# Kernel tuning notes

Hardware: AMD Instinct MI355X
Metric: run time of the kernel (lower is better)

The kernel has to match this reference:

```python
import jax, jax.numpy as jnp
import numpy as np

B, S, H = 64, 1024, 512
EPS = 1e-5


def layer_norm(x, g, b):
    mu = jnp.mean(x, axis=-1, keepdims=True)
    var = jnp.mean(jnp.square(x - mu), axis=-1, keepdims=True)
    return (x - mu) * jax.lax.rsqrt(var + EPS) * g + b


def lstm(x, w_ih, w_hh, b_ih, b_hh):
    # x: [B,S,H]; gates order (PyTorch): i, f, g, o; w_*: [4H, H]
    gx = jnp.einsum('bsh,gh->bsg', x, w_ih) + b_ih + b_hh  # [B,S,4H] one big GEMM
    gx = jnp.swapaxes(gx, 0, 1)  # time-major [S,B,4H]
    h0 = jnp.zeros((x.shape[0], w_hh.shape[1]), x.dtype)

    def step(carry, g_t):
        h, c = carry
        g = g_t + h @ w_hh.T
        i, f, gg, o = jnp.split(g, 4, axis=-1)
        c = jax.nn.sigmoid(f) * c + jax.nn.sigmoid(i) * jnp.tanh(gg)
        h = jax.nn.sigmoid(o) * jnp.tanh(c)
        return (h, c), h

    _, hs = jax.lax.scan(step, (h0, h0), gx)
    return jnp.swapaxes(hs, 0, 1)  # [B,S,H]


def setup_inputs() -> dict:
    key = jax.random.key(0)
    ks = jax.random.split(key, 12)
    s = 1.0 / np.sqrt(H)  # matches torch default uniform(-1/sqrt(H), 1/sqrt(H)) scale
    return {
        'x': jax.random.normal(ks[0], (B, S, H), jnp.float32),
        'pre_g': jnp.ones((H,), jnp.float32),
        'pre_b': jnp.zeros((H,), jnp.float32),
        'w_ih': jax.random.uniform(ks[1], (4 * H, H), jnp.float32, -s, s),
        'w_hh': jax.random.uniform(ks[2], (4 * H, H), jnp.float32, -s, s),
        'b_ih': jax.random.uniform(ks[3], (4 * H,), jnp.float32, -s, s),
        'b_hh': jax.random.uniform(ks[4], (4 * H,), jnp.float32, -s, s),
        'post_g': jnp.ones((H,), jnp.float32),
        'post_b': jnp.zeros((H,), jnp.float32),
        'w1': jax.random.uniform(ks[5], (H, 2 * H), jnp.float32, -s, s),
        'b1': jax.random.uniform(ks[6], (2 * H,), jnp.float32, -s, s),
        'w2': jax.random.uniform(ks[7], (2 * H, H), jnp.float32, -1.0 / np.sqrt(2 * H), 1.0 / np.sqrt(2 * H)),
        'b2': jax.random.uniform(ks[8], (H,), jnp.float32, -1.0 / np.sqrt(2 * H), 1.0 / np.sqrt(2 * H)),
    }


def reference(x, pre_g, pre_b, w_ih, w_hh, b_ih, b_hh, post_g, post_b, w1, b1, w2, b2):
    # Dropout is identity in eval mode.
    r = lstm(layer_norm(x, pre_g, pre_b), w_ih, w_hh, b_ih, b_hh)
    x = x + r
    h = layer_norm(x, post_g, post_b)
    h = jax.nn.gelu(h @ w1 + b1, approximate=False) @ w2 + b2
    return x + h
```

## Files before the change

### kernel.cpp

```cpp
#include <hip/hip_runtime.h>

typedef unsigned short u16;
typedef unsigned int   u32;
typedef unsigned long long u64;
typedef __attribute__((ext_vector_type(4))) float f32x4;
typedef __attribute__((ext_vector_type(8))) short short8;
typedef __attribute__((ext_vector_type(8))) __bf16 bf16x8v;
typedef __attribute__((ext_vector_type(4))) u32 u32x4;

__device__ __forceinline__ float bf2f(u16 v) { return __uint_as_float(((u32)v) << 16); }
__device__ __forceinline__ u16 f2bf(float f) {
    u32 u = __float_as_uint(f);
    u32 r = (u + 0x7fffu + ((u >> 16) & 1u)) >> 16;
    return (u16)r;
}
__device__ __forceinline__ float sigm(float x) { return 1.f / (1.f + __expf(-x)); }
__device__ __forceinline__ float tanh_f(float x) { return 1.f - 2.f / (__expf(2.f * x) + 1.f); }

template <class A>
__device__ __forceinline__ auto try_mfma(A a, A b, f32x4 c, int)
    -> decltype(__builtin_amdgcn_mfma_f32_16x16x32_bf16(a, b, c, 0, 0, 0)) {
    return __builtin_amdgcn_mfma_f32_16x16x32_bf16(a, b, c, 0, 0, 0);
}
template <class A>
__device__ __forceinline__ f32x4 try_mfma(A a, A b, f32x4 c, long) {
    return __builtin_amdgcn_mfma_f32_16x16x32_bf16(
        __builtin_bit_cast(bf16x8v, a), __builtin_bit_cast(bf16x8v, b), c, 0, 0, 0);
}
__device__ __forceinline__ f32x4 MFMA(short8 a, short8 b, f32x4 c) { return try_mfma(a, b, c, 0); }

__device__ __forceinline__ void cload4(const u32* p0, const u32* p1, const u32* p2, const u32* p3,
                                       u32x4& a, u32x4& b, u32x4& c, u32x4& d) {
    asm volatile("global_load_dwordx4 %0, %4, off sc0 sc1\n\t"
                 "global_load_dwordx4 %1, %5, off sc0 sc1\n\t"
                 "global_load_dwordx4 %2, %6, off sc0 sc1\n\t"
                 "global_load_dwordx4 %3, %7, off sc0 sc1\n\t"
                 "s_waitcnt vmcnt(0)"
                 : "=&v"(a), "=&v"(b), "=&v"(c), "=&v"(d)
                 : "v"(p0), "v"(p1), "v"(p2), "v"(p3)
                 : "memory");
}
__device__ __forceinline__ void cstore1(u32* p, u32 v) {
    asm volatile("global_store_dword %0, %1, off sc0 sc1" :: "v"(p), "v"(v) : "memory");
}


__global__ void k_prep(const float* __restrict__ w_ih, const float* __restrict__ w_hh,
                       const float* __restrict__ b_ih, const float* __restrict__ b_hh,
                       const float* __restrict__ w1, const float* __restrict__ w2,
                       u16* __restrict__ wihb, u16* __restrict__ whhb,
                       u16* __restrict__ w1t, u16* __restrict__ w2t, float* __restrict__ biasc) {
    for (u32 i = blockIdx.x * blockDim.x + threadIdx.x; i < 3147776u; i += gridDim.x * blockDim.x) {
        if (i < 1048576u) { wihb[i] = f2bf(w_ih[i]); }
        else if (i < 2097152u) { u32 j = i - 1048576u; whhb[j] = f2bf(w_hh[j]); }
        else if (i < 2621440u) { u32 j = i - 2097152u; u32 n = j >> 9,  k = j & 511u;  w1t[j] = f2bf(w1[k * 1024u + n]); }
        else if (i < 3145728u) { u32 j = i - 2621440u; u32 n = j >> 10, k = j & 1023u; w2t[j] = f2bf(w2[k * 512u + n]); }
        else { u32 j = i - 3145728u; biasc[j] = b_ih[j] + b_hh[j]; }
    }
}

__global__ void k_init(u32* __restrict__ h_ex) {
    u32 i = blockIdx.x * blockDim.x + threadIdx.x;
    if (i < 65536u) h_ex[i] = 0u;
}

__global__ __launch_bounds__(256) void k_pre_ln(const float* __restrict__ x,
                                                const float* __restrict__ g, const float* __restrict__ b,
                                                u16* __restrict__ out) {
    const int row = blockIdx.x * 4 + (threadIdx.x >> 6);
    const int lane = threadIdx.x & 63;
    const float* xr = x + (size_t)row * 512 + lane * 8;
    float v[8];
    *(float4*)(v)     = *(const float4*)(xr);
    *(float4*)(v + 4) = *(const float4*)(xr + 4);
    float s = 0.f, q = 0.f;
#pragma unroll
    for (int e = 0; e < 8; ++e) { s += v[e]; q += v[e] * v[e]; }
#pragma unroll
    for (int o = 32; o; o >>= 1) { s += __shfl_xor(s, o); q += __shfl_xor(q, o); }
    float mu = s * (1.f / 512.f);
    float rs = rsqrtf(q * (1.f / 512.f) - mu * mu + 1e-5f);
    short8 ov;
#pragma unroll
    for (int e = 0; e < 8; ++e) {
        int cidx = lane * 8 + e;
        ov[e] = (short)f2bf((v[e] - mu) * rs * g[cidx] + b[cidx]);
    }
    *(short8*)(out + (size_t)row * 512 + lane * 8) = ov;
}

__global__ __launch_bounds__(256) void k_res_ln(const float* __restrict__ x, const u16* __restrict__ r,
                                                const float* __restrict__ g, const float* __restrict__ b,
                                                u16* __restrict__ out) {
    const int row = blockIdx.x * 4 + (threadIdx.x >> 6);
    const int lane = threadIdx.x & 63;
    const float* xr = x + (size_t)row * 512 + lane * 8;
    short8 rv = *(const short8*)(r + (size_t)row * 512 + lane * 8);
    float v[8];
    *(float4*)(v)     = *(const float4*)(xr);
    *(float4*)(v + 4) = *(const float4*)(xr + 4);
#pragma unroll
    for (int e = 0; e < 8; ++e) v[e] += bf2f((u16)rv[e]);
    float s = 0.f, q = 0.f;
#pragma unroll
    for (int e = 0; e < 8; ++e) { s += v[e]; q += v[e] * v[e]; }
#pragma unroll
    for (int o = 32; o; o >>= 1) { s += __shfl_xor(s, o); q += __shfl_xor(q, o); }
    float mu = s * (1.f / 512.f);
    float rs = rsqrtf(q * (1.f / 512.f) - mu * mu + 1e-5f);
    short8 ov;
#pragma unroll
    for (int e = 0; e < 8; ++e) {
        int cidx = lane * 8 + e;
        ov[e] = (short)f2bf((v[e] - mu) * rs * g[cidx] + b[cidx]);
    }
    *(short8*)(out + (size_t)row * 512 + lane * 8) = ov;
}

template <int KD, int EPI>
__global__ __launch_bounds__(256, 2)
void k_gemm(const u16* __restrict__ A, const u16* __restrict__ B,
            const float* __restrict__ bias, u16* __restrict__ Cb, float* __restrict__ Cf,
            const float* __restrict__ Xres, const u16* __restrict__ Rres, int N) {
    __shared__ __align__(16) u16 At[128 * 64];
    __shared__ __align__(16) u16 Bt[128 * 64];
    const int tid = threadIdx.x;
    const int lane = tid & 63, wv = tid >> 6;
    const int m0 = blockIdx.y << 7, n0 = blockIdx.x << 7;
    const int wm = (wv >> 1) << 6, wn = (wv & 1) << 6;
    f32x4 acc[4][4] = {};
    const int r_st = tid >> 3, kb_st = tid & 7;

    for (int k0 = 0; k0 < KD; k0 += 64) {
#pragma unroll
        for (int rnd = 0; rnd < 4; ++rnd) {
            int rr = r_st + rnd * 32;
            short8 va = *(const short8*)(A + (size_t)(m0 + rr) * KD + (k0 + kb_st * 8));
            short8 vb = *(const short8*)(B + (size_t)(n0 + rr) * KD + (k0 + kb_st * 8));
            int byt = rr * 128 + ((kb_st * 16) ^ ((rr & 7) << 4));
            *(short8*)((char*)At + byt) = va;
            *(short8*)((char*)Bt + byt) = vb;
        }
        __syncthreads();
#pragma unroll
        for (int ks = 0; ks < 2; ++ks) {
            short8 af[4], bf[4];
#pragma unroll
            for (int mt = 0; mt < 4; ++mt) {
                int rowa = wm + mt * 16 + (lane & 15);
                int kba = ((lane >> 4) * 16 + ks * 64) ^ ((rowa & 7) << 4);
                af[mt] = *(const short8*)((const char*)At + rowa * 128 + kba);
                int rowb = wn + mt * 16 + (lane & 15);
                int kbb = ((lane >> 4) * 16 + ks * 64) ^ ((rowb & 7) << 4);
                bf[mt] = *(const short8*)((const char*)Bt + rowb * 128 + kbb);
            }
#pragma unroll
            for (int mt = 0; mt < 4; ++mt)
#pragma unroll
                for (int nt = 0; nt < 4; ++nt)
                    acc[mt][nt] = MFMA(af[mt], bf[nt], acc[mt][nt]);
        }
        __syncthreads();
    }
#pragma unroll
    for (int mt = 0; mt < 4; ++mt) {
#pragma unroll
        for (int nt = 0; nt < 4; ++nt) {
            int gn = n0 + wn + nt * 16 + (lane & 15);
            float bi = bias[gn];
#pragma unroll
            for (int i = 0; i < 4; ++i) {
                int gm = m0 + wm + mt * 16 + (lane >> 4) * 4 + i;
                float v = acc[mt][nt][i] + bi;
                size_t idx = (size_t)gm * (size_t)N + gn;
                if constexpr (EPI == 0) {
                    Cb[idx] = f2bf(v);
                } else if constexpr (EPI == 1) {
                    v = 0.5f * v * (1.f + erff(v * 0.70710678118f));
                    Cb[idx] = f2bf(v);
                } else {
                    Cf[idx] = v + Xres[idx] + bf2f(Rres[idx]);
                }
            }
        }
    }
}

__global__ __launch_bounds__(512, 1)
void k_scan(const u16* __restrict__ gx, const u16* __restrict__ whh,
            u16* __restrict__ rout, u32* __restrict__ h_ex) {
    const int grp = blockIdx.x >> 4, sl = blockIdx.x & 15;
    const int tid = threadIdx.x;
    const int lane = tid & 63, wv = tid >> 6;
    const int gt = wv >> 1, jb = wv & 1;
    const int cb = gt * 512 + sl * 32 + jb * 16;

    __shared__ __align__(16) u16 h_lds[16 * 512];
    __shared__ float g_buf[128 * 17];

    short8 wf[16];
    {
        const u16* wp = whh + (size_t)(cb + (lane & 15)) * 512 + (lane >> 4) * 8;
#pragma unroll
        for (int ks = 0; ks < 16; ++ks) wf[ks] = *(const short8*)(wp + ks * 32);
    }
    const int b_own = tid >> 5, jj = tid & 31;
    float cst = 0.f;
    u32* hex_g = h_ex + (u32)grp * 16384u;
    const int lc = gt * 32 + jb * 16 + (lane & 15);
    const int ngl = cb + (lane & 15);
    const u32 pub_idx = (u32)(b_own * 512 + sl * 32 + jj);

    const int jbyte = (tid & 127) * 8;
    char* ldst[4];
#pragma unroll
    for (int q = 0; q < 4; ++q) {
        int bq = q * 4 + (tid >> 7);
        ldst[q] = (char*)h_lds + bq * 1024 + (jbyte ^ ((bq & 7) << 4));
    }

    for (int t = 0; t < 1024; ++t) {
        float gxv[4];
#pragma unroll
        for (int i = 0; i < 4; ++i) {
            int bg = grp * 16 + (lane >> 4) * 4 + i;
            gxv[i] = bf2f(gx[((size_t)bg * 1024 + t) * 2048 + ngl]);
        }
        const u32* bse = hex_g + (u32)(t & 1) * 8192u + tid * 4;
        u32x4 qa, qb, qc, qd;
        for (;;) {
            cload4(bse, bse + 2048, bse + 4096, bse + 6144, qa, qb, qc, qd);
            u32 bad = 0;
#pragma unroll
            for (int e = 0; e < 4; ++e) {
                bad |= (qa[e] >> 16) ^ (u32)t;
                bad |= (qb[e] >> 16) ^ (u32)t;
                bad |= (qc[e] >> 16) ^ (u32)t;
                bad |= (qd[e] >> 16) ^ (u32)t;
            }
            if (!bad) break;
            __builtin_amdgcn_s_sleep(1);
        }
        {
            u64 p0 = (u64)(qa[0] & 0xffffu) | ((u64)(qa[1] & 0xffffu) << 16) |
                     ((u64)(qa[2] & 0xffffu) << 32) | ((u64)(qa[3] & 0xffffu) << 48);
            u64 p1 = (u64)(qb[0] & 0xffffu) | ((u64)(qb[1] & 0xffffu) << 16) |
                     ((u64)(qb[2] & 0xffffu) << 32) | ((u64)(qb[3] & 0xffffu) << 48);
            u64 p2 = (u64)(qc[0] & 0xffffu) | ((u64)(qc[1] & 0xffffu) << 16) |
                     ((u64)(qc[2] & 0xffffu) << 32) | ((u64)(qc[3] & 0xffffu) << 48);
            u64 p3 = (u64)(qd[0] & 0xffffu) | ((u64)(qd[1] & 0xffffu) << 16) |
                     ((u64)(qd[2] & 0xffffu) << 32) | ((u64)(qd[3] & 0xffffu) << 48);
            *(u64*)ldst[0] = p0;
            *(u64*)ldst[1] = p1;
            *(u64*)ldst[2] = p2;
            *(u64*)ldst[3] = p3;
        }
        __syncthreads();
        f32x4 a0 = {}, a1 = {}, a2 = {}, a3 = {};
        {
            const int rowa = lane & 15;
            const int kb0 = (lane >> 4) * 16;
            const int sw = (rowa & 7) << 4;
            const char* rb_ = (const char*)h_lds + rowa * 1024;
#pragma unroll
            for (int ks = 0; ks < 4; ++ks) {
                a0 = MFMA(*(const short8*)(rb_ + ((kb0 + (4 * ks + 0) * 64) ^ sw)), wf[4 * ks + 0], a0);
                a1 = MFMA(*(const short8*)(rb_ + ((kb0 + (4 * ks + 1) * 64) ^ sw)), wf[4 * ks + 1], a1);
                a2 = MFMA(*(const short8*)(rb_ + ((kb0 + (4 * ks + 2) * 64) ^ sw)), wf[4 * ks + 2], a2);
                a3 = MFMA(*(const short8*)(rb_ + ((kb0 + (4 * ks + 3) * 64) ^ sw)), wf[4 * ks + 3], a3);
            }
        }
        f32x4 acc = (a0 + a1) + (a2 + a3);
#pragma unroll
        for (int i = 0; i < 4; ++i)
            g_buf[lc * 17 + ((lane >> 4) * 4 + i)] = acc[i] + gxv[i];
        __syncthreads();
        {
            float iv = g_buf[jj * 17 + b_own];
            float fv = g_buf[(jj + 32) * 17 + b_own];
            float gv = g_buf[(jj + 64) * 17 + b_own];
            float ov = g_buf[(jj + 96) * 17 + b_own];
            cst = sigm(fv) * cst + sigm(iv) * tanh_f(gv);
            float h = sigm(ov) * tanh_f(cst);
            u16 hb = f2bf(h);
            u32* pp = hex_g + (u32)((t + 1) & 1) * 8192u + pub_idx;
            cstore1(pp, ((u32)(t + 1) << 16) | (u32)hb);
            rout[((size_t)(grp * 16 + b_own) * 1024 + t) * 512 + sl * 32 + jj] = hb;
        }
    }
}

extern "C" void kernel_launch(void* const* d_in, const int* in_sizes, int n_in,
                              void* d_out, int out_size, void* d_ws, size_t ws_size,
                              hipStream_t stream) {
    const float* x     = (const float*)d_in[0];
    const float* pre_g = (const float*)d_in[1];
    const float* pre_b = (const float*)d_in[2];
    const float* w_ih  = (const float*)d_in[3];
    const float* w_hh  = (const float*)d_in[4];
    const float* b_ih  = (const float*)d_in[5];
    const float* b_hh  = (const float*)d_in[6];
    const float* post_g= (const float*)d_in[7];
    const float* post_b= (const float*)d_in[8];
    const float* w1    = (const float*)d_in[9];
    const float* b1    = (const float*)d_in[10];
    const float* w2    = (const float*)d_in[11];
    const float* b2    = (const float*)d_in[12];
    float* out = (float*)d_out;

    char* p = (char*)d_ws;
    auto carve = [&](size_t bytes) { void* r = (void*)p; p += (bytes + 255) & ~(size_t)255; return r; };
    u16* xln   = (u16*)carve(64ull * 1024 * 512 * 2);
    u16* gxb   = (u16*)carve(64ull * 1024 * 2048 * 2);
    u16* rb    = (u16*)carve(64ull * 1024 * 512 * 2);
    u16* wihb  = (u16*)carve(2048ull * 512 * 2);
    u16* whhb  = (u16*)carve(2048ull * 512 * 2);
    u16* w1t   = (u16*)carve(1024ull * 512 * 2);
    u16* w2t   = (u16*)carve(512ull * 1024 * 2);
    float* biasc = (float*)carve(2048ull * 4);
    u32* h_ex  = (u32*)carve(65536ull * 4);
    u16* ln1 = xln;
    u16* h1  = gxb;

    k_prep<<<3072, 256, 0, stream>>>(w_ih, w_hh, b_ih, b_hh, w1, w2, wihb, whhb, w1t, w2t, biasc);
    k_init<<<256, 256, 0, stream>>>(h_ex);
    k_pre_ln<<<16384, 256, 0, stream>>>(x, pre_g, pre_b, xln);
    k_gemm<512, 0><<<dim3(16, 512), 256, 0, stream>>>(xln, wihb, biasc, gxb, nullptr, nullptr, nullptr, 2048);
    k_scan<<<64, 512, 0, stream>>>(gxb, whhb, rb, h_ex);
    k_res_ln<<<16384, 256, 0, stream>>>(x, rb, post_g, post_b, ln1);
    k_gemm<512, 1><<<dim3(8, 512), 256, 0, stream>>>(ln1, w1t, b1, h1, nullptr, nullptr, nullptr, 1024);
    k_gemm<1024, 2><<<dim3(4, 512), 256, 0, stream>>>(h1, w2t, b2, nullptr, out, x, rb, 512);
}
```

Measured before the change: 3.658 ms.

## Prefetch next-step gate inputs in LSTM loop and use direct global-to-LDS loads in GEMM

In the recurrent LSTM kernel, the input-projection values for step t+1 are loaded during step t and kept in registers, with the loop unrolled by two to ping-pong between buffers, so the global-load latency of gx stays off the serial critical path. The spin-wait now skips the sleep on its first retry, and the bf16 packing uses fewer 64-bit operations. The GEMM tile staging switches to the global_load_lds builtin, with the XOR swizzle moved into the source address, so data goes straight from global memory into shared memory without passing through registers. The last prefetch wraps to index 0 and loads a value that is never used, which is harmless, but the LDS swizzle mapping has to match the old layout exactly.

```diff
diff --git a/kernel.cpp b/kernel.cpp
--- a/kernel.cpp
+++ b/kernel.cpp
@@ -129,17 +129,17 @@
     const int m0 = blockIdx.y << 7, n0 = blockIdx.x << 7;
     const int wm = (wv >> 1) << 6, wn = (wv & 1) << 6;
     f32x4 acc[4][4] = {};
-    const int r_st = tid >> 3, kb_st = tid & 7;
+    const int rr = tid >> 3, kb = tid & 7;
+    const int ksw = (kb ^ (rr & 7)) * 8;
+    const int wvb = wv * 512;
 
     for (int k0 = 0; k0 < KD; k0 += 64) {
 #pragma unroll
-        for (int rnd = 0; rnd < 4; ++rnd) {
-            int rr = r_st + rnd * 32;
-            short8 va = *(const short8*)(A + (size_t)(m0 + rr) * KD + (k0 + kb_st * 8));
-            short8 vb = *(const short8*)(B + (size_t)(n0 + rr) * KD + (k0 + kb_st * 8));
-            int byt = rr * 128 + ((kb_st * 16) ^ ((rr & 7) << 4));
-            *(short8*)((char*)At + byt) = va;
-            *(short8*)((char*)Bt + byt) = vb;
+        for (int r = 0; r < 4; ++r) {
+            const u16* sa = A + (size_t)(m0 + r * 32 + rr) * KD + (k0 + ksw);
+            const u16* sb = B + (size_t)(n0 + r * 32 + rr) * KD + (k0 + ksw);
+            __builtin_amdgcn_global_load_lds((const u32*)sa, (u32*)&At[r * 2048 + wvb], 16, 0, 0);
+            __builtin_amdgcn_global_load_lds((const u32*)sb, (u32*)&Bt[r * 2048 + wvb], 16, 0, 0);
         }
         __syncthreads();
 #pragma unroll
@@ -218,16 +218,22 @@
         int bq = q * 4 + (tid >> 7);
         ldst[q] = (char*)h_lds + bq * 1024 + (jbyte ^ ((bq & 7) << 4));
     }
-
-    for (int t = 0; t < 1024; ++t) {
-        float gxv[4];
-#pragma unroll
-        for (int i = 0; i < 4; ++i) {
-            int bg = grp * 16 + (lane >> 4) * 4 + i;
-            gxv[i] = bf2f(gx[((size_t)bg * 1024 + t) * 2048 + ngl]);
-        }
+    const u16* gx_me = gx;
+    size_t gx_off[4];
+#pragma unroll
+    for (int i = 0; i < 4; ++i) {
+        int bg = grp * 16 + (lane >> 4) * 4 + i;
+        gx_off[i] = (size_t)bg * 1024 * 2048 + ngl;
+    }
+
+    u16 gxA[4], gxB[4];
+#pragma unroll
+    for (int i = 0; i < 4; ++i) gxA[i] = gx_me[gx_off[i]];
+
+    auto step = [&](int t, u16 (&cur)[4], u16 (&nxt)[4]) {
         const u32* bse = hex_g + (u32)(t & 1) * 8192u + tid * 4;
         u32x4 qa, qb, qc, qd;
+        int tries = 0;
         for (;;) {
             cload4(bse, bse + 2048, bse + 4096, bse + 6144, qa, qb, qc, qd);
             u32 bad = 0;
@@ -239,21 +245,22 @@
                 bad |= (qd[e] >> 16) ^ (u32)t;
             }
             if (!bad) break;
-            __builtin_amdgcn_s_sleep(1);
+            if (tries++) __builtin_amdgcn_s_sleep(1);
         }
         {
-            u64 p0 = (u64)(qa[0] & 0xffffu) | ((u64)(qa[1] & 0xffffu) << 16) |
-                     ((u64)(qa[2] & 0xffffu) << 32) | ((u64)(qa[3] & 0xffffu) << 48);
-            u64 p1 = (u64)(qb[0] & 0xffffu) | ((u64)(qb[1] & 0xffffu) << 16) |
-                     ((u64)(qb[2] & 0xffffu) << 32) | ((u64)(qb[3] & 0xffffu) << 48);
-            u64 p2 = (u64)(qc[0] & 0xffffu) | ((u64)(qc[1] & 0xffffu) << 16) |
-                     ((u64)(qc[2] & 0xffffu) << 32) | ((u64)(qc[3] & 0xffffu) << 48);
-            u64 p3 = (u64)(qd[0] & 0xffffu) | ((u64)(qd[1] & 0xffffu) << 16) |
-                     ((u64)(qd[2] & 0xffffu) << 32) | ((u64)(qd[3] & 0xffffu) << 48);
-            *(u64*)ldst[0] = p0;
-            *(u64*)ldst[1] = p1;
-            *(u64*)ldst[2] = p2;
-            *(u64*)ldst[3] = p3;
+            u32 a0 = (qa[0] & 0xffffu) | (qa[1] << 16), a1 = (qa[2] & 0xffffu) | (qa[3] << 16);
+            u32 b0 = (qb[0] & 0xffffu) | (qb[1] << 16), b1 = (qb[2] & 0xffffu) | (qb[3] << 16);
+            u32 c0 = (qc[0] & 0xffffu) | (qc[1] << 16), c1 = (qc[2] & 0xffffu) | (qc[3] << 16);
+            u32 d0 = (qd[0] & 0xffffu) | (qd[1] << 16), d1 = (qd[2] & 0xffffu) | (qd[3] << 16);
+            *(u64*)ldst[0] = (u64)a0 | ((u64)a1 << 32);
+            *(u64*)ldst[1] = (u64)b0 | ((u64)b1 << 32);
+            *(u64*)ldst[2] = (u64)c0 | ((u64)c1 << 32);
+            *(u64*)ldst[3] = (u64)d0 | ((u64)d1 << 32);
+        }
+        {
+            const u16* gp = gx_me + (size_t)(((t + 1) & 1023) * 2048);
+#pragma unroll
+            for (int i = 0; i < 4; ++i) nxt[i] = gp[gx_off[i]];
         }
         __syncthreads();
         f32x4 a0 = {}, a1 = {}, a2 = {}, a3 = {};
@@ -273,7 +280,7 @@
         f32x4 acc = (a0 + a1) + (a2 + a3);
 #pragma unroll
         for (int i = 0; i < 4; ++i)
-            g_buf[lc * 17 + ((lane >> 4) * 4 + i)] = acc[i] + gxv[i];
+            g_buf[lc * 17 + ((lane >> 4) * 4 + i)] = acc[i] + bf2f(cur[i]);
         __syncthreads();
         {
             float iv = g_buf[jj * 17 + b_own];
@@ -287,6 +294,11 @@
             cstore1(pp, ((u32)(t + 1) << 16) | (u32)hb);
             rout[((size_t)(grp * 16 + b_own) * 1024 + t) * 512 + sl * 32 + jj] = hb;
         }
+    };
+
+    for (int t = 0; t < 1024; t += 2) {
+        step(t, gxA, gxB);
+        step(t + 1, gxB, gxA);
     }
 }
 
```

Result: no change. 3.661 ms (+0.1%).
